# Kernel optimization log

Measured on AMD Instinct MI355X. Metric: run time of the kernel, lower is better.

Reference implementation:

```python
import jax, jax.numpy as jnp
import numpy as np

OUT_CHANNELS = 16
PH = PW = 7          # output_size
SR = 2               # sampling_ratio


def setup_inputs() -> dict:
    key = jax.random.key(0)
    k1, k2, k3, k4 = jax.random.split(key, 4)
    B, C, H, W = 4, OUT_CHANNELS * PH * PW, 80, 80
    feat = jax.random.normal(k1, (B, C, H, W), dtype=jnp.float32)
    N = 512
    bidx = jax.random.randint(k2, (N,), 0, B).astype(jnp.float32)
    tl = jax.random.uniform(k3, (N, 2), minval=0.0, maxval=0.7)   # x1, y1 (normalized)
    sz = jax.random.uniform(k4, (N, 2), minval=0.05, maxval=0.3)  # box size
    rois = jnp.concatenate([bidx[:, None], tl, tl + sz], axis=1)  # [N,5]
    return {"input": feat, "rois": rois}


def _psroi_one(feat_ps, roi):
    # feat_ps: [B, Co, PH, PW, H, W]  (position-sensitive channel layout)
    B, Co, _, _, H, W = feat_ps.shape
    f = feat_ps[roi[0].astype(jnp.int32)]              # [Co, PH, PW, H, W]
    x1 = roi[1] * W; y1 = roi[2] * H
    x2 = roi[3] * W; y2 = roi[4] * H                   # adaptive spatial_scale = (H, W)
    roi_h = jnp.maximum(y2 - y1, 0.1)
    roi_w = jnp.maximum(x2 - x1, 0.1)
    bin_h = roi_h / PH
    bin_w = roi_w / PW
    # sample coordinates per bin: [PH,SR] and [PW,SR]
    ys = y1 + jnp.arange(PH, dtype=f.dtype)[:, None] * bin_h + (jnp.arange(SR, dtype=f.dtype)[None, :] + 0.5) * bin_h / SR
    xs = x1 + jnp.arange(PW, dtype=f.dtype)[:, None] * bin_w + (jnp.arange(SR, dtype=f.dtype)[None, :] + 0.5) * bin_w / SR
    ym = (ys >= -1.0) & (ys <= H)
    xm = (xs >= -1.0) & (xs <= W)
    yc = jnp.clip(ys, 0.0, H - 1)
    xc = jnp.clip(xs, 0.0, W - 1)
    y0 = jnp.floor(yc).astype(jnp.int32)
    x0 = jnp.floor(xc).astype(jnp.int32)
    y1i = jnp.minimum(y0 + 1, H - 1)
    x1i = jnp.minimum(x0 + 1, W - 1)
    ly = yc - y0.astype(f.dtype); hy = 1.0 - ly        # [PH,SR]
    lx = xc - x0.astype(f.dtype); hx = 1.0 - lx        # [PW,SR]
    I = jnp.arange(PH)[:, None, None, None]            # bin row index
    J = jnp.arange(PW)[None, None, :, None]            # bin col index

    def g(Y, X):
        # gather f[c, i, j, Y[i,sy], X[j,sx]] -> [Co, PH, SR, PW, SR]
        return f[:, I, J, Y[:, :, None, None], X[None, None, :, :]]

    v = (g(y0, x0)  * (hy[:, :, None, None] * hx[None, None])
       + g(y0, x1i) * (hy[:, :, None, None] * lx[None, None])
       + g(y1i, x0) * (ly[:, :, None, None] * hx[None, None])
       + g(y1i, x1i) * (ly[:, :, None, None] * lx[None, None]))
    v = v * (ym[:, :, None, None] & xm[None, None]).astype(v.dtype)
    return v.mean(axis=(2, 4))                          # [Co, PH, PW]


def reference(input, rois):
    B, C, H, W = input.shape
    feat_ps = input.reshape(B, OUT_CHANNELS, PH, PW, H, W)
    rois = rois.reshape(-1, 5)
    out = jax.vmap(lambda r: _psroi_one(feat_ps, r))(rois)  # [N, Co, PH, PW]
    return out
```

## Files before the change

kernel.cpp:

```cpp
#include <hip/hip_runtime.h>

#define NB   4
#define CO   16
#define PH   7
#define PW   7
#define SR   2
#define HH   80
#define WW   80
#define NROI 512
#define CIJ  (CO*PH*PW)

typedef float f2v __attribute__((ext_vector_type(2), aligned(4)));
typedef float f4v __attribute__((ext_vector_type(4), aligned(4)));

__global__ __launch_bounds__(512) void psroi_align_kernel(
    const float* __restrict__ feat,
    const float* __restrict__ rois,
    float* __restrict__ out)
{
    int cij = blockIdx.x;
    int rem = cij % (PH * PW);
    int i = rem / PW;
    int j = rem % PW;
    int n = threadIdx.x;

    f4v r4 = *(const f4v*)(rois + n * 5);
    float r5 = rois[n * 5 + 4];
    int   b  = (int)r4.x;
    float x1 = r4.y * (float)WW;
    float y1 = r4.z * (float)HH;
    float x2 = r4.w * (float)WW;
    float y2 = r5   * (float)HH;

    float roi_h = fmaxf(y2 - y1, 0.1f);
    float roi_w = fmaxf(x2 - x1, 0.1f);
    float bin_h = roi_h * (1.0f / PH);
    float bin_w = roi_w * (1.0f / PW);

    const float* plane = feat + ((size_t)b * CIJ + (size_t)cij) * (HH * WW);

    float acc = 0.0f;
    #pragma unroll
    for (int sy = 0; sy < SR; ++sy) {
        float ys = y1 + (float)i * bin_h + ((float)sy + 0.5f) * bin_h / (float)SR;
        bool ymask = (ys >= -1.0f) && (ys <= (float)HH);
        float yc = fminf(fmaxf(ys, 0.0f), (float)(HH - 1));
        int   y0 = (int)floorf(yc);
        int   y1i = min(y0 + 1, HH - 1);
        float ly = yc - (float)y0;
        float hy = 1.0f - ly;

        #pragma unroll
        for (int sx = 0; sx < SR; ++sx) {
            float xs = x1 + (float)j * bin_w + ((float)sx + 0.5f) * bin_w / (float)SR;
            bool xmask = (xs >= -1.0f) && (xs <= (float)WW);
            float xc = fminf(fmaxf(xs, 0.0f), (float)(WW - 1));
            int   x0 = (int)floorf(xc);
            float lx = xc - (float)x0;
            float hx = 1.0f - lx;

            int x0c = min(x0, WW - 2);
            bool shifted = (x0 != x0c);

            f2v t  = *(const f2v*)(plane + y0  * WW + x0c);
            f2v bt = *(const f2v*)(plane + y1i * WW + x0c);

            float v00 = shifted ? t.y  : t.x;
            float v01 = t.y;
            float v10 = shifted ? bt.y : bt.x;
            float v11 = bt.y;

            float vtop = v00 * hx + v01 * lx;
            float vbot = v10 * hx + v11 * lx;
            float v = vtop * hy + vbot * ly;

            if (ymask && xmask) acc += v;
        }
    }

    out[(size_t)n * CIJ + cij] = acc * 0.25f;
}

extern "C" void kernel_launch(void* const* d_in, const int* in_sizes, int n_in,
                              void* d_out, int out_size, void* d_ws, size_t ws_size,
                              hipStream_t stream)
{
    const float* feat = (const float*)d_in[0];
    const float* rois = (const float*)d_in[1];
    float* out = (float*)d_out;

    psroi_align_kernel<<<CIJ, NROI, 0, stream>>>(feat, rois, out);
}
```

Before: 129.3 us.

## Stage each batch feature plane in shared memory before bilinear sampling

Each block now copies the 80x80 plane for its channel into LDS once per batch index, using coalesced vector loads, and the threads whose ROI belongs to that batch sample from LDS. This replaces scattered per-thread global gathers. In exchange every block reads all four batch planes in full, even those few ROIs touch, and adds barriers and 25KB of LDS per block, which may limit occupancy. Per-ROI coordinate setup is hoisted out of the batch loop.

New measurement: 115.1 us. 11.0% less time.

```diff
diff --git a/kernel.cpp b/kernel.cpp
--- a/kernel.cpp
+++ b/kernel.cpp
@@ -9,8 +9,8 @@
 #define WW   80
 #define NROI 512
 #define CIJ  (CO*PH*PW)
+#define PLANE (HH*WW)
 
-typedef float f2v __attribute__((ext_vector_type(2), aligned(4)));
 typedef float f4v __attribute__((ext_vector_type(4), aligned(4)));
 
 __global__ __launch_bounds__(512) void psroi_align_kernel(
@@ -18,63 +18,87 @@
     const float* __restrict__ rois,
     float* __restrict__ out)
 {
+    __shared__ float sp[PLANE];
+
     int cij = blockIdx.x;
     int rem = cij % (PH * PW);
     int i = rem / PW;
     int j = rem % PW;
     int n = threadIdx.x;
 
-    f4v r4 = *(const f4v*)(rois + n * 5);
-    float r5 = rois[n * 5 + 4];
-    int   b  = (int)r4.x;
-    float x1 = r4.y * (float)WW;
-    float y1 = r4.z * (float)HH;
-    float x2 = r4.w * (float)WW;
-    float y2 = r5   * (float)HH;
+    float rb = rois[n * 5 + 0];
+    float x1 = rois[n * 5 + 1] * (float)WW;
+    float y1 = rois[n * 5 + 2] * (float)HH;
+    float x2 = rois[n * 5 + 3] * (float)WW;
+    float y2 = rois[n * 5 + 4] * (float)HH;
+    int b = (int)rb;
 
     float roi_h = fmaxf(y2 - y1, 0.1f);
     float roi_w = fmaxf(x2 - x1, 0.1f);
     float bin_h = roi_h * (1.0f / PH);
     float bin_w = roi_w * (1.0f / PW);
 
-    const float* plane = feat + ((size_t)b * CIJ + (size_t)cij) * (HH * WW);
-
-    float acc = 0.0f;
+    int   p0r[SR], p1r[SR];
+    float lyv[SR], hyv[SR];
+    bool  ymv[SR];
     #pragma unroll
     for (int sy = 0; sy < SR; ++sy) {
         float ys = y1 + (float)i * bin_h + ((float)sy + 0.5f) * bin_h / (float)SR;
-        bool ymask = (ys >= -1.0f) && (ys <= (float)HH);
+        ymv[sy] = (ys >= -1.0f) && (ys <= (float)HH);
         float yc = fminf(fmaxf(ys, 0.0f), (float)(HH - 1));
         int   y0 = (int)floorf(yc);
         int   y1i = min(y0 + 1, HH - 1);
-        float ly = yc - (float)y0;
-        float hy = 1.0f - ly;
+        lyv[sy] = yc - (float)y0;
+        hyv[sy] = 1.0f - lyv[sy];
+        p0r[sy] = y0 * WW;
+        p1r[sy] = y1i * WW;
+    }
 
+    int   xcv[SR];
+    float lxv[SR], hxv[SR];
+    bool  xmv[SR], shv[SR];
+    #pragma unroll
+    for (int sx = 0; sx < SR; ++sx) {
+        float xs = x1 + (float)j * bin_w + ((float)sx + 0.5f) * bin_w / (float)SR;
+        xmv[sx] = (xs >= -1.0f) && (xs <= (float)WW);
+        float xc = fminf(fmaxf(xs, 0.0f), (float)(WW - 1));
+        int   x0 = (int)floorf(xc);
+        int   x0c = min(x0, WW - 2);
+        shv[sx] = (x0 != x0c);
+        lxv[sx] = xc - (float)x0;
+        hxv[sx] = 1.0f - lxv[sx];
+        xcv[sx] = x0c;
+    }
+
+    float acc = 0.0f;
+
+    for (int bb = 0; bb < NB; ++bb) {
+        const f4v* src = (const f4v*)(feat + ((size_t)bb * CIJ + (size_t)cij) * PLANE);
+        __syncthreads();
         #pragma unroll
-        for (int sx = 0; sx < SR; ++sx) {
-            float xs = x1 + (float)j * bin_w + ((float)sx + 0.5f) * bin_w / (float)SR;
-            bool xmask = (xs >= -1.0f) && (xs <= (float)WW);
-            float xc = fminf(fmaxf(xs, 0.0f), (float)(WW - 1));
-            int   x0 = (int)floorf(xc);
-            float lx = xc - (float)x0;
-            float hx = 1.0f - lx;
+        for (int it = 0; it < 4; ++it) {
+            int e = it * 512 + n;
+            if (e < PLANE / 4) ((f4v*)sp)[e] = src[e];
+        }
+        __syncthreads();
 
-            int x0c = min(x0, WW - 2);
-            bool shifted = (x0 != x0c);
-
-            f2v t  = *(const f2v*)(plane + y0  * WW + x0c);
-            f2v bt = *(const f2v*)(plane + y1i * WW + x0c);
-
-            float v00 = shifted ? t.y  : t.x;
-            float v01 = t.y;
-            float v10 = shifted ? bt.y : bt.x;
-            float v11 = bt.y;
-
-            float vtop = v00 * hx + v01 * lx;
-            float vbot = v10 * hx + v11 * lx;
-            float v = vtop * hy + vbot * ly;
-
-            if (ymask && xmask) acc += v;
+        if (b == bb) {
+            #pragma unroll
+            for (int sy = 0; sy < SR; ++sy) {
+                #pragma unroll
+                for (int sx = 0; sx < SR; ++sx) {
+                    int p0 = p0r[sy] + xcv[sx];
+                    int p1 = p1r[sy] + xcv[sx];
+                    float t0 = sp[p0], t1 = sp[p0 + 1];
+                    float b0 = sp[p1], b1 = sp[p1 + 1];
+                    float v00 = shv[sx] ? t1 : t0;
+                    float v10 = shv[sx] ? b1 : b0;
+                    float vtop = v00 * hxv[sx] + t1 * lxv[sx];
+                    float vbot = v10 * hxv[sx] + b1 * lxv[sx];
+                    float v = vtop * hyv[sy] + vbot * lyv[sy];
+                    if (ymv[sy] && xmv[sx]) acc += v;
+                }
+            }
         }
     }
 
```

## Stage feature planes in LDS and bucket ROIs by batch per block

Applied to the files above, without the earlier changes.

Each block, which owns one position-sensitive channel, now loads the full 80x80 plane for each batch index into shared memory with vectorized loads. It sorts ROIs by batch index in shared memory and lets only the threads whose ROI matches the current batch do the bilinear sampling from LDS. The next batch's plane is prefetched into registers while the current one is processed. This replaces scattered global gathers with coalesced bulk plane loads. The cost is that every block reads all four planes even when few ROIs use them, plus extra barriers, and most threads sit idle in each batch phase.

Result: faster. 114.2 us (-11.7%).

```diff
diff --git a/kernel.cpp b/kernel.cpp
--- a/kernel.cpp
+++ b/kernel.cpp
@@ -9,76 +9,114 @@
 #define WW   80
 #define NROI 512
 #define CIJ  (CO*PH*PW)
+#define PLANE (HH*WW)
+#define NF4  (PLANE/4)
 
-typedef float f2v __attribute__((ext_vector_type(2), aligned(4)));
-typedef float f4v __attribute__((ext_vector_type(4), aligned(4)));
+typedef float f4v __attribute__((ext_vector_type(4), aligned(16)));
 
-__global__ __launch_bounds__(512) void psroi_align_kernel(
+__global__ __launch_bounds__(512, 8) void psroi_align_kernel(
     const float* __restrict__ feat,
     const float* __restrict__ rois,
     float* __restrict__ out)
 {
+    __shared__ __align__(16) float sp[PLANE];
+    __shared__ unsigned short order[NROI];
+    __shared__ int cnt[NB];
+    __shared__ int base[NB + 1];
+
     int cij = blockIdx.x;
     int rem = cij % (PH * PW);
     int i = rem / PW;
     int j = rem % PW;
     int n = threadIdx.x;
 
-    f4v r4 = *(const f4v*)(rois + n * 5);
-    float r5 = rois[n * 5 + 4];
-    int   b  = (int)r4.x;
-    float x1 = r4.y * (float)WW;
-    float y1 = r4.z * (float)HH;
-    float x2 = r4.w * (float)WW;
-    float y2 = r5   * (float)HH;
+    if (n < NB) cnt[n] = 0;
+    __syncthreads();
+    int myb = (int)rois[n * 5 + 0];
+    int rank = atomicAdd(&cnt[myb], 1);
+    __syncthreads();
+    if (n == 0) {
+        base[0] = 0;
+        for (int k = 0; k < NB; ++k) base[k + 1] = base[k] + cnt[k];
+    }
+    __syncthreads();
+    order[base[myb] + rank] = (unsigned short)n;
 
-    float roi_h = fmaxf(y2 - y1, 0.1f);
-    float roi_w = fmaxf(x2 - x1, 0.1f);
-    float bin_h = roi_h * (1.0f / PH);
-    float bin_w = roi_w * (1.0f / PW);
-
-    const float* plane = feat + ((size_t)b * CIJ + (size_t)cij) * (HH * WW);
-
-    float acc = 0.0f;
-    #pragma unroll
-    for (int sy = 0; sy < SR; ++sy) {
-        float ys = y1 + (float)i * bin_h + ((float)sy + 0.5f) * bin_h / (float)SR;
-        bool ymask = (ys >= -1.0f) && (ys <= (float)HH);
-        float yc = fminf(fmaxf(ys, 0.0f), (float)(HH - 1));
-        int   y0 = (int)floorf(yc);
-        int   y1i = min(y0 + 1, HH - 1);
-        float ly = yc - (float)y0;
-        float hy = 1.0f - ly;
-
+    f4v regs[4];
+    {
+        const f4v* src = (const f4v*)(feat + (size_t)cij * PLANE);
         #pragma unroll
-        for (int sx = 0; sx < SR; ++sx) {
-            float xs = x1 + (float)j * bin_w + ((float)sx + 0.5f) * bin_w / (float)SR;
-            bool xmask = (xs >= -1.0f) && (xs <= (float)WW);
-            float xc = fminf(fmaxf(xs, 0.0f), (float)(WW - 1));
-            int   x0 = (int)floorf(xc);
-            float lx = xc - (float)x0;
-            float hx = 1.0f - lx;
-
-            int x0c = min(x0, WW - 2);
-            bool shifted = (x0 != x0c);
-
-            f2v t  = *(const f2v*)(plane + y0  * WW + x0c);
-            f2v bt = *(const f2v*)(plane + y1i * WW + x0c);
-
-            float v00 = shifted ? t.y  : t.x;
-            float v01 = t.y;
-            float v10 = shifted ? bt.y : bt.x;
-            float v11 = bt.y;
-
-            float vtop = v00 * hx + v01 * lx;
-            float vbot = v10 * hx + v11 * lx;
-            float v = vtop * hy + vbot * ly;
-
-            if (ymask && xmask) acc += v;
+        for (int it = 0; it < 4; ++it) {
+            int e = it * 512 + n;
+            if (e < NF4) regs[it] = src[e];
+        }
+        #pragma unroll
+        for (int it = 0; it < 4; ++it) {
+            int e = it * 512 + n;
+            if (e < NF4) ((f4v*)sp)[e] = regs[it];
         }
     }
 
-    out[(size_t)n * CIJ + cij] = acc * 0.25f;
+    for (int bb = 0; bb < NB; ++bb) {
+        if (bb + 1 < NB) {
+            const f4v* src = (const f4v*)(feat + ((size_t)(bb + 1) * CIJ + cij) * PLANE);
+            #pragma unroll
+            for (int it = 0; it < 4; ++it) {
+                int e = it * 512 + n;
+                if (e < NF4) regs[it] = src[e];
+            }
+        }
+        __syncthreads();
+
+        if (n >= base[bb] && n < base[bb + 1]) {
+            int m = order[n];
+            float x1 = rois[m * 5 + 1] * (float)WW;
+            float y1 = rois[m * 5 + 2] * (float)HH;
+            float x2 = rois[m * 5 + 3] * (float)WW;
+            float y2 = rois[m * 5 + 4] * (float)HH;
+            float bin_h = fmaxf(y2 - y1, 0.1f) * (1.0f / PH);
+            float bin_w = fmaxf(x2 - x1, 0.1f) * (1.0f / PW);
+
+            float acc = 0.0f;
+            #pragma unroll
+            for (int sy = 0; sy < SR; ++sy) {
+                float ys = y1 + (float)i * bin_h + ((float)sy + 0.5f) * bin_h / (float)SR;
+                bool ymask = (ys >= -1.0f) && (ys <= (float)HH);
+                float yc = fminf(fmaxf(ys, 0.0f), (float)(HH - 1));
+                int   y0 = (int)floorf(yc);
+                int   y1i = min(y0 + 1, HH - 1);
+                float ly = yc - (float)y0, hy = 1.0f - ly;
+                #pragma unroll
+                for (int sx = 0; sx < SR; ++sx) {
+                    float xs = x1 + (float)j * bin_w + ((float)sx + 0.5f) * bin_w / (float)SR;
+                    bool xmask = (xs >= -1.0f) && (xs <= (float)WW);
+                    float xc = fminf(fmaxf(xs, 0.0f), (float)(WW - 1));
+                    int   x0 = (int)floorf(xc);
+                    int   x0c = min(x0, WW - 2);
+                    bool  sh = (x0 != x0c);
+                    float lx = xc - (float)x0, hx = 1.0f - lx;
+
+                    float t0 = sp[y0  * WW + x0c], t1 = sp[y0  * WW + x0c + 1];
+                    float b0 = sp[y1i * WW + x0c], b1 = sp[y1i * WW + x0c + 1];
+
+                    float v00 = sh ? t1 : t0;
+                    float v10 = sh ? b1 : b0;
+                    float v = (v00 * hx + t1 * lx) * hy + (v10 * hx + b1 * lx) * ly;
+                    if (ymask && xmask) acc += v;
+                }
+            }
+            out[(size_t)m * CIJ + cij] = acc * 0.25f;
+        }
+
+        if (bb + 1 < NB) {
+            __syncthreads();
+            #pragma unroll
+            for (int it = 0; it < 4; ++it) {
+                int e = it * 512 + n;
+                if (e < NF4) ((f4v*)sp)[e] = regs[it];
+            }
+        }
+    }
 }
 
 extern "C" void kernel_launch(void* const* d_in, const int* in_sizes, int n_in,
```
